# Performance work log

Measured on AMD Instinct MI355X. Metric: run time of the kernel, lower is better.

The kernel has to match this reference:

```python
import jax, jax.numpy as jnp
import numpy as np

N_NODES = 100000
N_EDGES = 1600000
D_FEAT = 64
POS_DIM = 3
D_HID = 64


def setup_inputs() -> dict:
    key = jax.random.key(0)
    ks = jax.random.split(key, 8)
    s = lambda fan_in: 1.0 / np.sqrt(fan_in)
    x = jax.random.normal(ks[0], (N_NODES, D_FEAT), dtype=jnp.float32)
    pos = jax.random.normal(ks[1], (N_NODES, POS_DIM), dtype=jnp.float32)
    edge_index = jax.random.randint(ks[2], (2, N_EDGES), 0, N_NODES, dtype=jnp.int64)
    d_msg_in = 2 * D_FEAT + POS_DIM  # 131
    d_agg_in = 2 * D_FEAT            # 128
    return {
        "x": x,
        "edge_index": edge_index,
        "pos": pos,
        "mw1": jax.random.normal(ks[3], (d_msg_in, D_HID), dtype=jnp.float32) * s(d_msg_in),
        "mb1": jnp.zeros((D_HID,), dtype=jnp.float32),
        "mw2": jax.random.normal(ks[4], (D_HID, D_HID), dtype=jnp.float32) * s(D_HID),
        "mb2": jnp.zeros((D_HID,), dtype=jnp.float32),
        "aw1": jax.random.normal(ks[5], (d_agg_in, D_HID), dtype=jnp.float32) * s(d_agg_in),
        "ab1": jnp.zeros((D_HID,), dtype=jnp.float32),
        "aw2": jax.random.normal(ks[6], (D_HID, D_HID), dtype=jnp.float32) * s(D_HID),
        "ab2": jnp.zeros((D_HID,), dtype=jnp.float32),
    }


def reference(x, edge_index, pos, mw1, mb1, mw2, mb2, aw1, ab1, aw2, ab2):
    # flow='target_to_source': aggregation node i = edge_index[0], neighbor j = edge_index[1]
    i = edge_index[0]
    j = edge_index[1]
    # message: msg_net(cat[x_i, x_j, pos_j - pos_i])   [E, 2d+pos]
    inp = jnp.concatenate([x[i], x[j], pos[j] - pos[i]], axis=1)
    h = jax.nn.relu(inp @ mw1 + mb1)
    msg = h @ mw2 + mb2  # [E, D_HID]
    n = x.shape[0]
    # scatter-mean aggregate at node i
    msg_sum = jax.ops.segment_sum(msg, i, num_segments=n)
    cnt = jax.ops.segment_sum(jnp.ones((i.shape[0], 1), x.dtype), i, num_segments=n)
    aggr = msg_sum / jnp.maximum(cnt, 1.0)
    # update: aggr_net(cat[x, aggr])  (self_val=True)
    u = jnp.concatenate([x, aggr], axis=1)
    return jax.nn.relu(u @ aw1 + ab1) @ aw2 + ab2
```

## Files before the change

kernel.cpp:

```cpp
#include <hip/hip_runtime.h>
#include <hip/hip_fp16.h>

#define N_NODES 100000
#define N_EDGES 1600000
#define NPART 98
#define CAP   20480

typedef _Float16 half8 __attribute__((ext_vector_type(8)));
typedef float f32x4 __attribute__((ext_vector_type(4)));

#define WS_OFF   0
#define WS_PCUR  400016
#define WS_B     400528
#define WS_SJ    401040
#define WS_WCOMB 6801040
#define WS_BCOMB 6817424
#define WS_PK    6817680
#define WS_QI8   6858640
#define WS_QS    13258640
#define WS_BIN   19658640
#define WS_HM16  19658640

__global__ void k_init0(int* pcur) {
    int t = threadIdx.x;
    if (t < NPART) pcur[t] = t * CAP;
}

__global__ void __launch_bounds__(256) k_binc(const int* __restrict__ ei,
                                              const int* __restrict__ ej,
                                              int* pcur, int* __restrict__ binned) {
    __shared__ int cnt[NPART];
    __shared__ int base[NPART];
    int t = threadIdx.x;
    for (int q = t; q < NPART; q += 256) cnt[q] = 0;
    __syncthreads();

    int e0 = blockIdx.x * 2048 + t * 4;
    int e1 = e0 + 1024;
    bool v0 = e0 < N_EDGES, v1 = e1 < N_EDGES;
    int4 i0, j0, i1, j1;
    int p0[4], s0[4], p1[4], s1[4];
    if (v0) {
        i0 = *(const int4*)(ei + e0); j0 = *(const int4*)(ej + e0);
        p0[0] = i0.x >> 10; s0[0] = atomicAdd(&cnt[p0[0]], 1);
        p0[1] = i0.y >> 10; s0[1] = atomicAdd(&cnt[p0[1]], 1);
        p0[2] = i0.z >> 10; s0[2] = atomicAdd(&cnt[p0[2]], 1);
        p0[3] = i0.w >> 10; s0[3] = atomicAdd(&cnt[p0[3]], 1);
    }
    if (v1) {
        i1 = *(const int4*)(ei + e1); j1 = *(const int4*)(ej + e1);
        p1[0] = i1.x >> 10; s1[0] = atomicAdd(&cnt[p1[0]], 1);
        p1[1] = i1.y >> 10; s1[1] = atomicAdd(&cnt[p1[1]], 1);
        p1[2] = i1.z >> 10; s1[2] = atomicAdd(&cnt[p1[2]], 1);
        p1[3] = i1.w >> 10; s1[3] = atomicAdd(&cnt[p1[3]], 1);
    }
    __syncthreads();
    for (int q = t; q < NPART; q += 256)
        base[q] = cnt[q] ? atomicAdd(&pcur[q], cnt[q]) : 0;
    __syncthreads();
    if (v0) {
        int a;
        a = base[p0[0]] + s0[0]; if (a < (p0[0] + 1) * CAP) binned[a] = ((i0.x & 1023) << 17) | j0.x;
        a = base[p0[1]] + s0[1]; if (a < (p0[1] + 1) * CAP) binned[a] = ((i0.y & 1023) << 17) | j0.y;
        a = base[p0[2]] + s0[2]; if (a < (p0[2] + 1) * CAP) binned[a] = ((i0.z & 1023) << 17) | j0.z;
        a = base[p0[3]] + s0[3]; if (a < (p0[3] + 1) * CAP) binned[a] = ((i0.w & 1023) << 17) | j0.w;
    }
    if (v1) {
        int a;
        a = base[p1[0]] + s1[0]; if (a < (p1[0] + 1) * CAP) binned[a] = ((i1.x & 1023) << 17) | j1.x;
        a = base[p1[1]] + s1[1]; if (a < (p1[1] + 1) * CAP) binned[a] = ((i1.y & 1023) << 17) | j1.y;
        a = base[p1[2]] + s1[2]; if (a < (p1[2] + 1) * CAP) binned[a] = ((i1.z & 1023) << 17) | j1.z;
        a = base[p1[3]] + s1[3]; if (a < (p1[3] + 1) * CAP) binned[a] = ((i1.w & 1023) << 17) | j1.w;
    }
}

__global__ void k_scanB(const int* __restrict__ pcur, int* B) {
    __shared__ int s[128];
    int t = threadIdx.x;
    int c = 0;
    if (t < NPART) c = min(pcur[t] - t * CAP, CAP);
    s[t] = c;
    __syncthreads();
    for (int o = 1; o < 128; o <<= 1) {
        int a = (t >= o) ? s[t - o] : 0;
        __syncthreads();
        s[t] += a;
        __syncthreads();
    }
    if (t < NPART) B[t] = s[t] - c;
    if (t == NPART - 1) B[NPART] = s[t];
}

__global__ void __launch_bounds__(256) k_fill3(const int* __restrict__ binned,
                                               const int* __restrict__ B,
                                               int* __restrict__ off,
                                               int* __restrict__ sj) {
    __shared__ int hist[1024];
    __shared__ int tsum[256];
    int p = blockIdx.x, t = threadIdx.x;
    int b0g = B[p];
    int cnt_p = B[p + 1] - b0g;
    const int* src = binned + p * CAP;

    #pragma unroll
    for (int q = 0; q < 4; ++q) hist[t * 4 + q] = 0;
    __syncthreads();
    for (int e = t; e < cnt_p; e += 256) atomicAdd(&hist[src[e] >> 17], 1);
    __syncthreads();

    int b0 = hist[t * 4], b1 = hist[t * 4 + 1], b2 = hist[t * 4 + 2], b3 = hist[t * 4 + 3];
    int c1 = b0, c2 = c1 + b1, c3 = c2 + b2, tot = c3 + b3;
    tsum[t] = tot;
    __syncthreads();
    for (int o = 1; o < 256; o <<= 1) {
        int a = (t >= o) ? tsum[t - o] : 0;
        __syncthreads();
        tsum[t] += a;
        __syncthreads();
    }
    int tex = tsum[t] - tot;
    hist[t * 4]     = tex;
    hist[t * 4 + 1] = tex + c1;
    hist[t * 4 + 2] = tex + c2;
    hist[t * 4 + 3] = tex + c3;
    __syncthreads();

    int lo = p * 1024;
    #pragma unroll
    for (int q = 0; q < 4; ++q) {
        int n = t * 4 + q, g = lo + n;
        if (g < N_NODES) off[g] = b0g + hist[n];
    }
    if (p == NPART - 1 && t == 0) off[N_NODES] = B[NPART];
    __syncthreads();

    for (int e = t; e < cnt_p; e += 256) {
        int v = src[e];
        int slot = atomicAdd(&hist[v >> 17], 1);
        sj[b0g + slot] = v & 0x1FFFF;
    }
}

__global__ void k_wcomb(const float* __restrict__ mw2, const float* __restrict__ mb2,
                        const float* __restrict__ aw1, float* wcomb, float* bcomb) {
    int o = blockIdx.x * blockDim.x + threadIdx.x;
    if (o < 64 * 64) {
        int c = o >> 6, k = o & 63;
        float s = 0.f;
        #pragma unroll 8
        for (int a = 0; a < 64; ++a) s += mw2[c * 64 + a] * aw1[(64 + a) * 64 + k];
        wcomb[o] = s;
    } else if (o < 64 * 64 + 64) {
        int k = o - 64 * 64;
        float s = 0.f;
        #pragma unroll 8
        for (int a = 0; a < 64; ++a) s += mb2[a] * aw1[(64 + a) * 64 + k];
        bcomb[k] = s;
    }
}

__global__ void k_wpack(const float* __restrict__ mw1, const float* __restrict__ aw1,
                        const float* __restrict__ wcomb, const float* __restrict__ aw2,
                        _Float16* __restrict__ pk) {
    int mat = blockIdx.x;
    const float* src = (mat == 0) ? mw1 : (mat == 1) ? (mw1 + 4096)
                     : (mat == 2) ? aw1 : (mat == 3) ? wcomb : aw2;
    _Float16* dst = pk + mat * 4096;
    for (int t = threadIdx.x; t < 4096; t += 256) {
        int b_ = t & 7, l = (t >> 3) & 63, z = t >> 9;
        int kg = z & 1, nt = z >> 1;
        int k = kg * 32 + ((l >> 4) << 3) + b_;
        int n = nt * 16 + (l & 15);
        dst[t] = (_Float16)src[k * 64 + n];
    }
}

__device__ __forceinline__ half8 afrag_f32(const float* src, int row, int kg, int l) {
    const float* p = src + (size_t)row * 64 + kg * 32 + ((l >> 4) << 3);
    float4 u = *(const float4*)p;
    float4 v = *(const float4*)(p + 4);
    half8 h;
    h[0] = (_Float16)u.x; h[1] = (_Float16)u.y; h[2] = (_Float16)u.z; h[3] = (_Float16)u.w;
    h[4] = (_Float16)v.x; h[5] = (_Float16)v.y; h[6] = (_Float16)v.z; h[7] = (_Float16)v.w;
    return h;
}

__global__ void __launch_bounds__(256) k_pre(const float* __restrict__ x,
                                             const float* __restrict__ pos,
                                             const float* __restrict__ mw1,
                                             const float* __restrict__ mb1,
                                             const _Float16* __restrict__ pk,
                                             float* __restrict__ P,
                                             signed char* __restrict__ Qi8,
                                             float* __restrict__ Qs) {
    int w = threadIdx.x >> 6, l = threadIdx.x & 63;
    int m0 = blockIdx.x * 128 + w * 32;

    half8 a[2][2];
    #pragma unroll
    for (int s = 0; s < 2; ++s)
        #pragma unroll
        for (int kg = 0; kg < 2; ++kg) {
            int row = m0 + s * 16 + (l & 15);
            if (row >= N_NODES) row = N_NODES - 1;
            a[s][kg] = afrag_f32(x, row, kg, l);
        }

    f32x4 z = {0.f, 0.f, 0.f, 0.f};
    f32x4 accP[2][4], accQ[2][4];
    #pragma unroll
    for (int s = 0; s < 2; ++s)
        #pragma unroll
        for (int nt = 0; nt < 4; ++nt) { accP[s][nt] = z; accQ[s][nt] = z; }

    #pragma unroll
    for (int nt = 0; nt < 4; ++nt)
        #pragma unroll
        for (int kg = 0; kg < 2; ++kg) {
            half8 b = *(const half8*)(pk + ((nt * 2 + kg) * 64 + l) * 8);
            accP[0][nt] = __builtin_amdgcn_mfma_f32_16x16x32_f16(a[0][kg], b, accP[0][nt], 0, 0, 0);
            accP[1][nt] = __builtin_amdgcn_mfma_f32_16x16x32_f16(a[1][kg], b, accP[1][nt], 0, 0, 0);
        }
    const _Float16* pkb = pk + 4096;
    #pragma unroll
    for (int nt = 0; nt < 4; ++nt)
        #pragma unroll
        for (int kg = 0; kg < 2; ++kg) {
            half8 b = *(const half8*)(pkb + ((nt * 2 + kg) * 64 + l) * 8);
            accQ[0][nt] = __builtin_amdgcn_mfma_f32_16x16x32_f16(a[0][kg], b, accQ[0][nt], 0, 0, 0);
            accQ[1][nt] = __builtin_amdgcn_mfma_f32_16x16x32_f16(a[1][kg], b, accQ[1][nt], 0, 0, 0);
        }

    int col = l & 15;
    float wx[4], wy[4], wz[4], bb[4];
    #pragma unroll
    for (int nt = 0; nt < 4; ++nt) {
        int n = nt * 16 + col;
        wx[nt] = mw1[128 * 64 + n];
        wy[nt] = mw1[129 * 64 + n];
        wz[nt] = mw1[130 * 64 + n];
        bb[nt] = mb1[n];
    }
    #pragma unroll
    for (int s = 0; s < 2; ++s)
        #pragma unroll
        for (int r = 0; r < 4; ++r) {
            int m = m0 + s * 16 + ((l >> 4) << 2) + r;
            if (m >= N_NODES) continue;
            float px = pos[3 * m], py = pos[3 * m + 1], pz = pos[3 * m + 2];
            float qn[4];
            #pragma unroll
            for (int nt = 0; nt < 4; ++nt) {
                int n = nt * 16 + col;
                float pd = px * wx[nt] + py * wy[nt] + pz * wz[nt];
                P[(size_t)m * 64 + n] = accP[s][nt][r] + bb[nt] - pd;
                qn[nt] = accQ[s][nt][r] + pd;
            }
            float mx = fmaxf(fmaxf(fabsf(qn[0]), fabsf(qn[1])),
                             fmaxf(fabsf(qn[2]), fabsf(qn[3])));
            #pragma unroll
            for (int d = 1; d < 16; d <<= 1) mx = fmaxf(mx, __shfl_xor(mx, d, 64));
            float inv = (mx > 0.f) ? 127.f / mx : 0.f;
            #pragma unroll
            for (int nt = 0; nt < 4; ++nt)
                Qi8[(size_t)m * 64 + nt * 16 + col] = (signed char)(int)rintf(qn[nt] * inv);
            if (col == 0) Qs[m] = mx * (1.f / 127.f);
        }
}

__global__ void __launch_bounds__(256) k_c1(const signed char* __restrict__ Qi8,
                                            const float* __restrict__ Qs,
                                            const int* __restrict__ off,
                                            const int* __restrict__ sj,
                                            const float* __restrict__ Phm,
                                            _Float16* __restrict__ hm16) {
    int wave = threadIdx.x >> 6, lane = threadIdx.x & 63;
    int node = blockIdx.x * 4 + wave;
    if (node >= N_NODES) return;
    float Pv = Phm[(size_t)node * 64 + lane];
    int o0 = off[node], o1 = off[node + 1];
    int dg = o1 - o0;
    float acc = 0.f;
    for (int base = o0; base < o1; base += 64) {
        int m = min(64, o1 - base);
        int jvv = (lane < m) ? sj[base + lane] : 0;
        for (int g = 0; g < 64; g += 16) {
            if (g >= m) break;
            float bv[16], sv[16];
            #pragma unroll
            for (int cc = 0; cc < 16; ++cc) {
                int jc = __builtin_amdgcn_readlane(jvv, g + cc);
                sv[cc] = Qs[jc];
                bv[cc] = (float)Qi8[jc * 64 + lane];
            }
            #pragma unroll
            for (int cc = 0; cc < 16; ++cc) {
                float r = fmaxf(fmaf(bv[cc], sv[cc], Pv), 0.f);
                acc += (g + cc < m) ? r : 0.f;
            }
        }
    }
    hm16[(size_t)node * 64 + lane] = (_Float16)((dg > 0) ? acc / (float)dg : 0.f);
}

__global__ void __launch_bounds__(256) k_c2(const float* __restrict__ x,
                                            const _Float16* __restrict__ hm16,
                                            const _Float16* __restrict__ pk,
                                            const float* __restrict__ ab1,
                                            const float* __restrict__ bcomb,
                                            const float* __restrict__ ab2,
                                            const int* __restrict__ off,
                                            float* __restrict__ out) {
    __shared__ _Float16 lsh[4][2][16][64];
    int w = threadIdx.x >> 6, l = threadIdx.x & 63;
    int m0 = blockIdx.x * 128 + w * 32;
    int col = l & 15;

    f32x4 z = {0.f, 0.f, 0.f, 0.f};
    f32x4 acc[2][4];
    #pragma unroll
    for (int s = 0; s < 2; ++s)
        #pragma unroll
        for (int nt = 0; nt < 4; ++nt) acc[s][nt] = z;

    {
        half8 a[2][2];
        #pragma unroll
        for (int s = 0; s < 2; ++s)
            #pragma unroll
            for (int kg = 0; kg < 2; ++kg) {
                int row = m0 + s * 16 + (l & 15);
                if (row >= N_NODES) row = N_NODES - 1;
                a[s][kg] = afrag_f32(x, row, kg, l);
            }
        const _Float16* pk1 = pk + 2 * 4096;
        #pragma unroll
        for (int nt = 0; nt < 4; ++nt)
            #pragma unroll
            for (int kg = 0; kg < 2; ++kg) {
                half8 b = *(const half8*)(pk1 + ((nt * 2 + kg) * 64 + l) * 8);
                acc[0][nt] = __builtin_amdgcn_mfma_f32_16x16x32_f16(a[0][kg], b, acc[0][nt], 0, 0, 0);
                acc[1][nt] = __builtin_amdgcn_mfma_f32_16x16x32_f16(a[1][kg], b, acc[1][nt], 0, 0, 0);
            }
    }
    {
        half8 a[2][2];
        #pragma unroll
        for (int s = 0; s < 2; ++s)
            #pragma unroll
            for (int kg = 0; kg < 2; ++kg) {
                int row = m0 + s * 16 + (l & 15);
                if (row >= N_NODES) row = N_NODES - 1;
                a[s][kg] = *(const half8*)(hm16 + (size_t)row * 64 + kg * 32 + ((l >> 4) << 3));
            }
        const _Float16* pk2 = pk + 3 * 4096;
        #pragma unroll
        for (int nt = 0; nt < 4; ++nt)
            #pragma unroll
            for (int kg = 0; kg < 2; ++kg) {
                half8 b = *(const half8*)(pk2 + ((nt * 2 + kg) * 64 + l) * 8);
                acc[0][nt] = __builtin_amdgcn_mfma_f32_16x16x32_f16(a[0][kg], b, acc[0][nt], 0, 0, 0);
                acc[1][nt] = __builtin_amdgcn_mfma_f32_16x16x32_f16(a[1][kg], b, acc[1][nt], 0, 0, 0);
            }
    }

    float a1n[4], bcn[4];
    #pragma unroll
    for (int nt = 0; nt < 4; ++nt) {
        int n = nt * 16 + col;
        a1n[nt] = ab1[n];
        bcn[nt] = bcomb[n];
    }
    #pragma unroll
    for (int s = 0; s < 2; ++s)
        #pragma unroll
        for (int r = 0; r < 4; ++r) {
            int row = ((l >> 4) << 2) + r;
            int m = m0 + s * 16 + row;
            int dg = (m < N_NODES) ? (off[m + 1] - off[m]) : 0;
            #pragma unroll
            for (int nt = 0; nt < 4; ++nt) {
                int n = nt * 16 + col;
                float v = acc[s][nt][r] + a1n[nt] + ((dg > 0) ? bcn[nt] : 0.f);
                v = fmaxf(v, 0.f);
                lsh[w][s][row][n ^ ((row & 7) << 3)] = (_Float16)v;
            }
        }
    __syncthreads();

    f32x4 acc2[2][4];
    #pragma unroll
    for (int s = 0; s < 2; ++s)
        #pragma unroll
        for (int nt = 0; nt < 4; ++nt) acc2[s][nt] = z;
    {
        half8 a[2][2];
        #pragma unroll
        for (int s = 0; s < 2; ++s)
            #pragma unroll
            for (int kg = 0; kg < 2; ++kg) {
                int rr = l & 15;
                int c0 = (kg * 32 + ((l >> 4) << 3)) ^ ((rr & 7) << 3);
                a[s][kg] = *(const half8*)&lsh[w][s][rr][c0];
            }
        const _Float16* pk3 = pk + 4 * 4096;
        #pragma unroll
        for (int nt = 0; nt < 4; ++nt)
            #pragma unroll
            for (int kg = 0; kg < 2; ++kg) {
                half8 b = *(const half8*)(pk3 + ((nt * 2 + kg) * 64 + l) * 8);
                acc2[0][nt] = __builtin_amdgcn_mfma_f32_16x16x32_f16(a[0][kg], b, acc2[0][nt], 0, 0, 0);
                acc2[1][nt] = __builtin_amdgcn_mfma_f32_16x16x32_f16(a[1][kg], b, acc2[1][nt], 0, 0, 0);
            }
    }

    float a2n[4];
    #pragma unroll
    for (int nt = 0; nt < 4; ++nt) a2n[nt] = ab2[nt * 16 + col];
    #pragma unroll
    for (int s = 0; s < 2; ++s)
        #pragma unroll
        for (int r = 0; r < 4; ++r) {
            int m = m0 + s * 16 + ((l >> 4) << 2) + r;
            if (m >= N_NODES) continue;
            #pragma unroll
            for (int nt = 0; nt < 4; ++nt)
                out[(size_t)m * 64 + nt * 16 + col] = acc2[s][nt][r] + a2n[nt];
        }
}

extern "C" void kernel_launch(void* const* d_in, const int* in_sizes, int n_in,
                              void* d_out, int out_size, void* d_ws, size_t ws_size,
                              hipStream_t stream) {
    const float* x   = (const float*)d_in[0];
    const int*   ei  = (const int*)d_in[1];
    const int*   ej  = ((const int*)d_in[1]) + N_EDGES;
    const float* pos = (const float*)d_in[2];
    const float* mw1 = (const float*)d_in[3];
    const float* mb1 = (const float*)d_in[4];
    const float* mw2 = (const float*)d_in[5];
    const float* mb2 = (const float*)d_in[6];
    const float* aw1 = (const float*)d_in[7];
    const float* ab1 = (const float*)d_in[8];
    const float* aw2 = (const float*)d_in[9];
    const float* ab2 = (const float*)d_in[10];

    char* ws = (char*)d_ws;
    int*         off    = (int*)(ws + WS_OFF);
    int*         pcur   = (int*)(ws + WS_PCUR);
    int*         B      = (int*)(ws + WS_B);
    int*         sj     = (int*)(ws + WS_SJ);
    float*       wcomb  = (float*)(ws + WS_WCOMB);
    float*       bcomb  = (float*)(ws + WS_BCOMB);
    _Float16*    pk     = (_Float16*)(ws + WS_PK);
    signed char* Qi8    = (signed char*)(ws + WS_QI8);
    float*       Qs     = (float*)(ws + WS_QS);
    int*         binned = (int*)(ws + WS_BIN);
    _Float16*    hm16   = (_Float16*)(ws + WS_HM16);
    float*       out    = (float*)d_out;

    const int NBT = (N_NODES + 127) / 128;
    const int NBB = (N_EDGES + 2047) / 2048;
    hipLaunchKernelGGL(k_init0, dim3(1), dim3(128), 0, stream, pcur);
    hipLaunchKernelGGL(k_binc,  dim3(NBB), dim3(256), 0, stream, ei, ej, pcur, binned);
    hipLaunchKernelGGL(k_scanB, dim3(1), dim3(128), 0, stream, pcur, B);
    hipLaunchKernelGGL(k_fill3, dim3(NPART), dim3(256), 0, stream, binned, B, off, sj);
    hipLaunchKernelGGL(k_wcomb, dim3(17), dim3(256), 0, stream, mw2, mb2, aw1, wcomb, bcomb);
    hipLaunchKernelGGL(k_wpack, dim3(5), dim3(256), 0, stream, mw1, aw1, wcomb, aw2, pk);
    hipLaunchKernelGGL(k_pre,   dim3(NBT), dim3(256), 0, stream, x, pos, mw1, mb1, pk, out, Qi8, Qs);
    hipLaunchKernelGGL(k_c1,    dim3((N_NODES + 3) / 4), dim3(256), 0, stream,
                       Qi8, Qs, off, sj, out, hm16);
    hipLaunchKernelGGL(k_c2,    dim3(NBT), dim3(256), 0, stream,
                       x, hm16, pk, ab1, bcomb, ab2, off, out);
}
```

Baseline: 179.8 us.

## Enlarge binning blocks to two-pass count/scatter and process two nodes per wave

The binning kernel now handles 8192 edges per block in two passes: first it counts partitions from the source indices, then it re-reads the edges and scatters them using shared-memory cursors. This cuts global atomics on the partition cursors and the number of blocks, at the cost of reading the source indices twice. The gather kernel k_c1 now has each wave interleave two nodes so more independent gather loads are in flight to hide latency. It adds an occupancy hint and drops the bounds check, relying on N_NODES dividing evenly by 8.

```diff
diff --git a/kernel.cpp b/kernel.cpp
--- a/kernel.cpp
+++ b/kernel.cpp
@@ -5,6 +5,7 @@
 #define N_EDGES 1600000
 #define NPART 98
 #define CAP   20480
+#define EB    8192
 
 typedef _Float16 half8 __attribute__((ext_vector_type(8)));
 typedef float f32x4 __attribute__((ext_vector_type(4)));
@@ -30,47 +31,42 @@
                                               const int* __restrict__ ej,
                                               int* pcur, int* __restrict__ binned) {
     __shared__ int cnt[NPART];
-    __shared__ int base[NPART];
+    __shared__ int wcur[NPART];
     int t = threadIdx.x;
     for (int q = t; q < NPART; q += 256) cnt[q] = 0;
     __syncthreads();
-
-    int e0 = blockIdx.x * 2048 + t * 4;
-    int e1 = e0 + 1024;
-    bool v0 = e0 < N_EDGES, v1 = e1 < N_EDGES;
-    int4 i0, j0, i1, j1;
-    int p0[4], s0[4], p1[4], s1[4];
-    if (v0) {
-        i0 = *(const int4*)(ei + e0); j0 = *(const int4*)(ej + e0);
-        p0[0] = i0.x >> 10; s0[0] = atomicAdd(&cnt[p0[0]], 1);
-        p0[1] = i0.y >> 10; s0[1] = atomicAdd(&cnt[p0[1]], 1);
-        p0[2] = i0.z >> 10; s0[2] = atomicAdd(&cnt[p0[2]], 1);
-        p0[3] = i0.w >> 10; s0[3] = atomicAdd(&cnt[p0[3]], 1);
-    }
-    if (v1) {
-        i1 = *(const int4*)(ei + e1); j1 = *(const int4*)(ej + e1);
-        p1[0] = i1.x >> 10; s1[0] = atomicAdd(&cnt[p1[0]], 1);
-        p1[1] = i1.y >> 10; s1[1] = atomicAdd(&cnt[p1[1]], 1);
-        p1[2] = i1.z >> 10; s1[2] = atomicAdd(&cnt[p1[2]], 1);
-        p1[3] = i1.w >> 10; s1[3] = atomicAdd(&cnt[p1[3]], 1);
+    int base_e = blockIdx.x * EB;
+    #pragma unroll 2
+    for (int it = 0; it < EB / 1024; ++it) {
+        int e = base_e + it * 1024 + t * 4;
+        if (e < N_EDGES) {
+            int4 iv = *(const int4*)(ei + e);
+            atomicAdd(&cnt[iv.x >> 10], 1);
+            atomicAdd(&cnt[iv.y >> 10], 1);
+            atomicAdd(&cnt[iv.z >> 10], 1);
+            atomicAdd(&cnt[iv.w >> 10], 1);
+        }
     }
     __syncthreads();
     for (int q = t; q < NPART; q += 256)
-        base[q] = cnt[q] ? atomicAdd(&pcur[q], cnt[q]) : 0;
-    __syncthreads();
-    if (v0) {
-        int a;
-        a = base[p0[0]] + s0[0]; if (a < (p0[0] + 1) * CAP) binned[a] = ((i0.x & 1023) << 17) | j0.x;
-        a = base[p0[1]] + s0[1]; if (a < (p0[1] + 1) * CAP) binned[a] = ((i0.y & 1023) << 17) | j0.y;
-        a = base[p0[2]] + s0[2]; if (a < (p0[2] + 1) * CAP) binned[a] = ((i0.z & 1023) << 17) | j0.z;
-        a = base[p0[3]] + s0[3]; if (a < (p0[3] + 1) * CAP) binned[a] = ((i0.w & 1023) << 17) | j0.w;
-    }
-    if (v1) {
-        int a;
-        a = base[p1[0]] + s1[0]; if (a < (p1[0] + 1) * CAP) binned[a] = ((i1.x & 1023) << 17) | j1.x;
-        a = base[p1[1]] + s1[1]; if (a < (p1[1] + 1) * CAP) binned[a] = ((i1.y & 1023) << 17) | j1.y;
-        a = base[p1[2]] + s1[2]; if (a < (p1[2] + 1) * CAP) binned[a] = ((i1.z & 1023) << 17) | j1.z;
-        a = base[p1[3]] + s1[3]; if (a < (p1[3] + 1) * CAP) binned[a] = ((i1.w & 1023) << 17) | j1.w;
+        wcur[q] = cnt[q] ? atomicAdd(&pcur[q], cnt[q]) : 0;
+    __syncthreads();
+    #pragma unroll 2
+    for (int it = 0; it < EB / 1024; ++it) {
+        int e = base_e + it * 1024 + t * 4;
+        if (e < N_EDGES) {
+            int4 iv = *(const int4*)(ei + e);
+            int4 jv = *(const int4*)(ej + e);
+            int a, p;
+            p = iv.x >> 10; a = atomicAdd(&wcur[p], 1);
+            if (a < (p + 1) * CAP) binned[a] = ((iv.x & 1023) << 17) | jv.x;
+            p = iv.y >> 10; a = atomicAdd(&wcur[p], 1);
+            if (a < (p + 1) * CAP) binned[a] = ((iv.y & 1023) << 17) | jv.y;
+            p = iv.z >> 10; a = atomicAdd(&wcur[p], 1);
+            if (a < (p + 1) * CAP) binned[a] = ((iv.z & 1023) << 17) | jv.z;
+            p = iv.w >> 10; a = atomicAdd(&wcur[p], 1);
+            if (a < (p + 1) * CAP) binned[a] = ((iv.w & 1023) << 17) | jv.w;
+        }
     }
 }
 
@@ -268,39 +264,64 @@
         }
 }
 
-__global__ void __launch_bounds__(256) k_c1(const signed char* __restrict__ Qi8,
-                                            const float* __restrict__ Qs,
-                                            const int* __restrict__ off,
-                                            const int* __restrict__ sj,
-                                            const float* __restrict__ Phm,
-                                            _Float16* __restrict__ hm16) {
+__global__ void __launch_bounds__(256, 4) k_c1(const signed char* __restrict__ Qi8,
+                                               const float* __restrict__ Qs,
+                                               const int* __restrict__ off,
+                                               const int* __restrict__ sj,
+                                               const float* __restrict__ Phm,
+                                               _Float16* __restrict__ hm16) {
     int wave = threadIdx.x >> 6, lane = threadIdx.x & 63;
-    int node = blockIdx.x * 4 + wave;
-    if (node >= N_NODES) return;
-    float Pv = Phm[(size_t)node * 64 + lane];
-    int o0 = off[node], o1 = off[node + 1];
-    int dg = o1 - o0;
-    float acc = 0.f;
-    for (int base = o0; base < o1; base += 64) {
-        int m = min(64, o1 - base);
-        int jvv = (lane < m) ? sj[base + lane] : 0;
+    int n0 = blockIdx.x * 8 + wave * 2;
+    float Pv0 = Phm[(size_t)n0 * 64 + lane];
+    float Pv1 = Phm[(size_t)(n0 + 1) * 64 + lane];
+    int oA = off[n0], oM = off[n0 + 1], oE = off[n0 + 2];
+    int dgA = oM - oA, dgB = oE - oM;
+    float accA = 0.f, accB = 0.f;
+    int eA = oA, eB = oM;
+    while (eA < oM || eB < oE) {
+        int mA = min(64, oM - eA);
+        int mB = min(64, oE - eB);
+        int jvA = (lane < mA) ? sj[eA + lane] : 0;
+        int jvB = (lane < mB) ? sj[eB + lane] : 0;
         for (int g = 0; g < 64; g += 16) {
-            if (g >= m) break;
-            float bv[16], sv[16];
-            #pragma unroll
-            for (int cc = 0; cc < 16; ++cc) {
-                int jc = __builtin_amdgcn_readlane(jvv, g + cc);
-                sv[cc] = Qs[jc];
-                bv[cc] = (float)Qi8[jc * 64 + lane];
-            }
-            #pragma unroll
-            for (int cc = 0; cc < 16; ++cc) {
-                float r = fmaxf(fmaf(bv[cc], sv[cc], Pv), 0.f);
-                acc += (g + cc < m) ? r : 0.f;
-            }
-        }
-    }
-    hm16[(size_t)node * 64 + lane] = (_Float16)((dg > 0) ? acc / (float)dg : 0.f);
+            if (g >= mA && g >= mB) break;
+            float vA[16], sA[16], vB[16], sB[16];
+            if (g < mA) {
+                #pragma unroll
+                for (int cc = 0; cc < 16; ++cc) {
+                    int jc = __builtin_amdgcn_readlane(jvA, g + cc);
+                    sA[cc] = Qs[jc];
+                    vA[cc] = (float)Qi8[jc * 64 + lane];
+                }
+            }
+            if (g < mB) {
+                #pragma unroll
+                for (int cc = 0; cc < 16; ++cc) {
+                    int jc = __builtin_amdgcn_readlane(jvB, g + cc);
+                    sB[cc] = Qs[jc];
+                    vB[cc] = (float)Qi8[jc * 64 + lane];
+                }
+            }
+            if (g < mA) {
+                #pragma unroll
+                for (int cc = 0; cc < 16; ++cc) {
+                    float r = fmaxf(fmaf(vA[cc], sA[cc], Pv0), 0.f);
+                    accA += (g + cc < mA) ? r : 0.f;
+                }
+            }
+            if (g < mB) {
+                #pragma unroll
+                for (int cc = 0; cc < 16; ++cc) {
+                    float r = fmaxf(fmaf(vB[cc], sB[cc], Pv1), 0.f);
+                    accB += (g + cc < mB) ? r : 0.f;
+                }
+            }
+        }
+        eA += mA;
+        eB += mB;
+    }
+    hm16[(size_t)n0 * 64 + lane]       = (_Float16)((dgA > 0) ? accA / (float)dgA : 0.f);
+    hm16[(size_t)(n0 + 1) * 64 + lane] = (_Float16)((dgB > 0) ? accB / (float)dgB : 0.f);
 }
 
 __global__ void __launch_bounds__(256) k_c2(const float* __restrict__ x,
@@ -460,7 +481,7 @@
     float*       out    = (float*)d_out;
 
     const int NBT = (N_NODES + 127) / 128;
-    const int NBB = (N_EDGES + 2047) / 2048;
+    const int NBB = (N_EDGES + EB - 1) / EB;
     hipLaunchKernelGGL(k_init0, dim3(1), dim3(128), 0, stream, pcur);
     hipLaunchKernelGGL(k_binc,  dim3(NBB), dim3(256), 0, stream, ei, ej, pcur, binned);
     hipLaunchKernelGGL(k_scanB, dim3(1), dim3(128), 0, stream, pcur, B);
@@ -468,7 +489,7 @@
     hipLaunchKernelGGL(k_wcomb, dim3(17), dim3(256), 0, stream, mw2, mb2, aw1, wcomb, bcomb);
     hipLaunchKernelGGL(k_wpack, dim3(5), dim3(256), 0, stream, mw1, aw1, wcomb, aw2, pk);
     hipLaunchKernelGGL(k_pre,   dim3(NBT), dim3(256), 0, stream, x, pos, mw1, mb1, pk, out, Qi8, Qs);
-    hipLaunchKernelGGL(k_c1,    dim3((N_NODES + 3) / 4), dim3(256), 0, stream,
+    hipLaunchKernelGGL(k_c1,    dim3(N_NODES / 8), dim3(256), 0, stream,
                        Qi8, Qs, off, sj, out, hm16);
     hipLaunchKernelGGL(k_c2,    dim3(NBT), dim3(256), 0, stream,
                        x, hm16, pk, ab1, bcomb, ab2, off, out);
```

Result: faster. 176.2 us (-2.0%).
